# Kernel optimization log

Hardware: AMD Instinct MI355X
Metric: run time of the kernel (lower is better)

Reference implementation:

```python
import jax, jax.numpy as jnp
import numpy as np

B, T, I, H = 8192, 658, 7, 1
D1, D2, D3 = 1024, 512, 128


def setup_inputs() -> dict:
    key = jax.random.key(0)
    ks = jax.random.split(key, 14)
    return {
        "x": jax.random.normal(ks[0], (B, T, I), dtype=jnp.float32),
        "h0": jax.random.uniform(ks[1], (1, B, H), dtype=jnp.float32),
        "W_ih": jax.random.normal(ks[2], (H, I), dtype=jnp.float32) * 0.3,
        "W_hh": jax.random.normal(ks[3], (H, H), dtype=jnp.float32) * 0.3,
        "b_ih": jax.random.normal(ks[4], (H,), dtype=jnp.float32) * 0.1,
        "b_hh": jax.random.normal(ks[5], (H,), dtype=jnp.float32) * 0.1,
        "w1": jax.random.normal(ks[6], (D1, T), dtype=jnp.float32) * 0.03,
        "b1": jax.random.normal(ks[7], (D1,), dtype=jnp.float32) * 0.01,
        "w2": jax.random.normal(ks[8], (D2, D1), dtype=jnp.float32) * 0.03,
        "b2": jax.random.normal(ks[9], (D2,), dtype=jnp.float32) * 0.01,
        "w3": jax.random.normal(ks[10], (D3, D2), dtype=jnp.float32) * 0.03,
        "b3": jax.random.normal(ks[11], (D3,), dtype=jnp.float32) * 0.01,
        "w4": jax.random.normal(ks[12], (T, D3), dtype=jnp.float32) * 0.03,
        "b4": jax.random.normal(ks[13], (T,), dtype=jnp.float32) * 0.01,
    }


def _forward(x, h0, W_ih, W_hh, b_ih, b_hh, w1, b1, w2, b2, w3, b3, w4, b4):
    # Precompute input projection for all timesteps: [T, B, H]
    xw = jnp.einsum("bti,hi->tbh", x, W_ih) + b_ih

    def step(h, xw_t):  # h: [B, H]
        h_new = jnp.tanh(xw_t + h @ W_hh.T + b_hh)
        return h_new, h_new

    h_last, hs = jax.lax.scan(step, h0[0], xw)  # hs: [T, B, H]
    out = jnp.transpose(hs, (1, 0, 2)).reshape(-1, T)  # [B, T] (view(-1, seq))

    out = jax.nn.relu(out @ w1.T + b1)
    out = jax.nn.relu(out @ w2.T + b2)
    out = jax.nn.relu(out @ w3.T + b3)
    out = out @ w4.T + b4
    return out, h_last[None]  # hidden: [1, B, H]


def reference(x, h0, W_ih, W_hh, b_ih, b_hh, w1, b1, w2, b2, w3, b3, w4, b4):
    return _forward(x, h0, W_ih, W_hh, b_ih, b_hh, w1, b1, w2, b2, w3, b3, w4, b4)
```

## Files before the change

### kernel.cpp

```cpp
#include <hip/hip_runtime.h>
#include <hip/hip_bf16.h>
#include <stdint.h>
#include <stddef.h>

#define B_  8192
#define T_  658
#define I_  7
#define TP  672
#define D1_ 1024
#define D2_ 512
#define D3_ 128
#define NP4 768

#define NB  64
#define CT  32
#define NCH 21

#define XWBLKS 21504
#define CVBLKS 5376

typedef __bf16 bf16x8 __attribute__((ext_vector_type(8)));
typedef float  floatx4 __attribute__((ext_vector_type(4)));

__device__ __forceinline__ void gload_lds16(const void* g, void* l) {
    __builtin_amdgcn_global_load_lds(
        (const __attribute__((address_space(1))) void*)g,
        (__attribute__((address_space(3))) void*)l, 16, 0, 0);
}

__device__ __forceinline__ unsigned int pack_bf16x2(float a, float b) {
    unsigned int ua = __float_as_uint(a);
    unsigned int ub = __float_as_uint(b);
    ua += 0x7fffu + ((ua >> 16) & 1u);
    ub += 0x7fffu + ((ub >> 16) & 1u);
    return (ua >> 16) | (ub & 0xffff0000u);
}

__device__ __forceinline__ float bf16lo(unsigned int u) { return __uint_as_float(u << 16); }
__device__ __forceinline__ float bf16hi(unsigned int u) { return __uint_as_float(u & 0xffff0000u); }

__global__ void xw_conv_kernel(const float* __restrict__ x,
                               const float* __restrict__ Wih,
                               const float* __restrict__ bih,
                               __bf16* __restrict__ xwb,
                               const float* __restrict__ w1, const float* __restrict__ w2,
                               const float* __restrict__ w3, const float* __restrict__ w4,
                               __bf16* __restrict__ w1b, __bf16* __restrict__ w2b,
                               __bf16* __restrict__ w3b, __bf16* __restrict__ w4b) {
    if (blockIdx.x < XWBLKS) {
        const int i = blockIdx.x * 256 + threadIdx.x;
        const int b = i / TP, t = i - b * TP;
        float s = 0.0f;
        if (t < T_) {
            const float* xp = x + ((size_t)b * T_ + t) * I_;
            s = bih[0];
#pragma unroll
            for (int j = 0; j < I_; ++j) s = fmaf(xp[j], Wih[j], s);
        }
        xwb[i] = (__bf16)s;
        return;
    }
    int i = (blockIdx.x - XWBLKS) * 256 + threadIdx.x;
    if (i < D1_ * TP) {
        int r = i / TP, c = i - r * TP;
        w1b[i] = (__bf16)(c < T_ ? w1[r * T_ + c] : 0.0f);
        return;
    }
    i -= D1_ * TP;
    if (i < D2_ * D1_) { w2b[i] = (__bf16)w2[i]; return; }
    i -= D2_ * D1_;
    if (i < D3_ * D2_) { w3b[i] = (__bf16)w3[i]; return; }
    i -= D3_ * D2_;
    {
        int r = i / D3_, c = i - r * D3_;
        w4b[i] = (__bf16)(r < T_ ? w4[r * D3_ + c] : 0.0f);
    }
}

__global__ __launch_bounds__(64) void scan_kernel(
    const __bf16* __restrict__ xwb, const float* __restrict__ h0,
    const float* __restrict__ Whh, const float* __restrict__ bhh,
    __bf16* __restrict__ A0, float* __restrict__ hlast) {
    __shared__ float        lds_x[CT * (NB + 1)];
    __shared__ unsigned int lds_o[NB * 17];

    const int tid = threadIdx.x;
    const int b0 = blockIdx.x * NB;
    const float whh = Whh[0], bh = bhh[0];
    const float C2L = 2.8853900817779268f;
    const float whhc = whh * C2L;
    float h = h0[b0 + tid];

    uint4 pf[4];
    unsigned int res[CT / 2];

#pragma unroll
    for (int l = 0; l < 4; ++l) {
        const int idx = l * NB + tid;
        const int bl = idx >> 2, q = idx & 3;
        pf[l] = *(const uint4*)(xwb + (size_t)(b0 + bl) * TP + q * 8);
    }

    for (int c = 0; c < NCH; ++c) {
        const int t0 = c * CT;
        __syncthreads();
#pragma unroll
        for (int l = 0; l < 4; ++l) {
            const int idx = l * NB + tid;
            const int bl = idx >> 2, q = idx & 3;
            const uint4 v = pf[l];
            lds_x[(q * 8 + 0) * (NB + 1) + bl] = bf16lo(v.x);
            lds_x[(q * 8 + 1) * (NB + 1) + bl] = bf16hi(v.x);
            lds_x[(q * 8 + 2) * (NB + 1) + bl] = bf16lo(v.y);
            lds_x[(q * 8 + 3) * (NB + 1) + bl] = bf16hi(v.y);
            lds_x[(q * 8 + 4) * (NB + 1) + bl] = bf16lo(v.z);
            lds_x[(q * 8 + 5) * (NB + 1) + bl] = bf16hi(v.z);
            lds_x[(q * 8 + 6) * (NB + 1) + bl] = bf16lo(v.w);
            lds_x[(q * 8 + 7) * (NB + 1) + bl] = bf16hi(v.w);
        }
        if (c > 0) {
#pragma unroll
            for (int j = 0; j < 16; ++j) lds_o[tid * 17 + j] = res[j];
        }
        __syncthreads();
        if (c > 0) {
            const int tprev = t0 - CT;
#pragma unroll
            for (int l = 0; l < 4; ++l) {
                const int idx = l * NB + tid;
                const int bl = idx >> 2, q = idx & 3;
                uint4 v;
                v.x = lds_o[bl * 17 + q * 4 + 0];
                v.y = lds_o[bl * 17 + q * 4 + 1];
                v.z = lds_o[bl * 17 + q * 4 + 2];
                v.w = lds_o[bl * 17 + q * 4 + 3];
                *(uint4*)(A0 + (size_t)(b0 + bl) * TP + tprev + q * 8) = v;
            }
        }
        if (c + 1 < NCH) {
            const int tn = t0 + CT;
#pragma unroll
            for (int l = 0; l < 4; ++l) {
                const int idx = l * NB + tid;
                const int bl = idx >> 2, q = idx & 3;
                pf[l] = *(const uint4*)(xwb + (size_t)(b0 + bl) * TP + tn + q * 8);
            }
        }
        if (c < NCH - 1) {
#pragma unroll
            for (int k = 0; k < CT; k += 2) {
                float xv0 = lds_x[k * (NB + 1) + tid];
                float xv1 = lds_x[(k + 1) * (NB + 1) + tid];
                float e0 = __builtin_amdgcn_exp2f(fmaf(h, whhc, (xv0 + bh) * C2L));
                h = fmaf(-2.0f, __builtin_amdgcn_rcpf(e0 + 1.0f), 1.0f);
                float r0 = h;
                float e1 = __builtin_amdgcn_exp2f(fmaf(h, whhc, (xv1 + bh) * C2L));
                h = fmaf(-2.0f, __builtin_amdgcn_rcpf(e1 + 1.0f), 1.0f);
                res[k >> 1] = pack_bf16x2(r0, h);
            }
        } else {
            const int nval = T_ - t0;
#pragma unroll
            for (int k = 0; k < CT; k += 2) {
                float r0 = 0.0f, r1 = 0.0f;
                if (k < nval) {
                    float xv0 = lds_x[k * (NB + 1) + tid];
                    float e0 = __builtin_amdgcn_exp2f(fmaf(h, whhc, (xv0 + bh) * C2L));
                    h = fmaf(-2.0f, __builtin_amdgcn_rcpf(e0 + 1.0f), 1.0f);
                    r0 = h;
                }
                if (k + 1 < nval) {
                    float xv1 = lds_x[(k + 1) * (NB + 1) + tid];
                    float e1 = __builtin_amdgcn_exp2f(fmaf(h, whhc, (xv1 + bh) * C2L));
                    h = fmaf(-2.0f, __builtin_amdgcn_rcpf(e1 + 1.0f), 1.0f);
                    r1 = h;
                }
                res[k >> 1] = pack_bf16x2(r0, r1);
            }
        }
    }
    __syncthreads();
#pragma unroll
    for (int j = 0; j < 16; ++j) lds_o[tid * 17 + j] = res[j];
    __syncthreads();
    {
        const int tprev = TP - CT;
#pragma unroll
        for (int l = 0; l < 4; ++l) {
            const int idx = l * NB + tid;
            const int bl = idx >> 2, q = idx & 3;
            uint4 v;
            v.x = lds_o[bl * 17 + q * 4 + 0];
            v.y = lds_o[bl * 17 + q * 4 + 1];
            v.z = lds_o[bl * 17 + q * 4 + 2];
            v.w = lds_o[bl * 17 + q * 4 + 3];
            *(uint4*)(A0 + (size_t)(b0 + bl) * TP + tprev + q * 8) = v;
        }
    }
    hlast[b0 + tid] = h;
}

template<int BM, int BN>
__global__ __launch_bounds__(256, 4) void gemm_bt(
    const __bf16* __restrict__ A, const __bf16* __restrict__ W,
    const float* __restrict__ bias, __bf16* __restrict__ outb,
    float* __restrict__ outf, int K, int Npad, int Nreal, int relu) {
    constexpr int MI = BM / 32;
    constexpr int NJ = BN / 32;
    constexpr int nA = BM / 64;
    constexpr int nB = BN / 64;
    __shared__ __align__(16) __bf16 As[BM * 32];
    __shared__ __align__(16) __bf16 Bs[BN * 32];

    const int tid = threadIdx.x;
    const int m0 = blockIdx.x * BM, n0 = blockIdx.y * BN;
    const int lane = tid & 63, wave = tid >> 6;
    const int wm = (wave & 1) * (BM / 2), wn = (wave >> 1) * (BN / 2);
    const int quad = lane >> 4, l16 = lane & 15;

    const int eoff = tid * 8;
    const int rowS = eoff >> 5;
    const int colS = eoff & 31;
    const __bf16* gaa[nA];
    const __bf16* gbb[nB];
    __bf16* laa[nA];
    __bf16* lbb[nB];
#pragma unroll
    for (int c = 0; c < nA; ++c) {
        gaa[c] = A + (size_t)(m0 + rowS + c * 64) * K + colS;
        laa[c] = As + c * 2048 + (tid & 192) * 8;
    }
#pragma unroll
    for (int c = 0; c < nB; ++c) {
        gbb[c] = W + (size_t)(n0 + rowS + c * 64) * K + colS;
        lbb[c] = Bs + c * 2048 + (tid & 192) * 8;
    }

    floatx4 acc[MI][NJ] = {};

    for (int k0 = 0; k0 < K; k0 += 32) {
#pragma unroll
        for (int c = 0; c < nA; ++c) gload_lds16(gaa[c] + k0, laa[c]);
#pragma unroll
        for (int c = 0; c < nB; ++c) gload_lds16(gbb[c] + k0, lbb[c]);
        __syncthreads();

        bf16x8 af[MI], bg[NJ];
#pragma unroll
        for (int i = 0; i < MI; ++i)
            af[i] = *(const bf16x8*)(As + (wm + i * 16 + l16) * 32 + quad * 8);
#pragma unroll
        for (int j = 0; j < NJ; ++j)
            bg[j] = *(const bf16x8*)(Bs + (wn + j * 16 + l16) * 32 + quad * 8);
#pragma unroll
        for (int i = 0; i < MI; ++i)
#pragma unroll
            for (int j = 0; j < NJ; ++j)
                acc[i][j] = __builtin_amdgcn_mfma_f32_16x16x32_bf16(af[i], bg[j], acc[i][j], 0, 0, 0);
        __syncthreads();
    }

#pragma unroll
    for (int j = 0; j < NJ; ++j) {
        const int n = n0 + wn + j * 16 + l16;
        const float bv = (n < Nreal) ? bias[n] : 0.0f;
#pragma unroll
        for (int i = 0; i < MI; ++i) {
#pragma unroll
            for (int r = 0; r < 4; ++r) {
                const int m = m0 + wm + i * 16 + quad * 4 + r;
                float v = acc[i][j][r] + bv;
                if (relu) v = fmaxf(v, 0.0f);
                if (outb) {
                    outb[(size_t)m * Npad + n] = (__bf16)v;
                } else if (n < Nreal) {
                    outf[(size_t)m * Nreal + n] = v;
                }
            }
        }
    }
}

extern "C" void kernel_launch(void* const* d_in, const int* in_sizes, int n_in,
                              void* d_out, int out_size, void* d_ws, size_t ws_size,
                              hipStream_t stream) {
    const float* x   = (const float*)d_in[0];
    const float* h0  = (const float*)d_in[1];
    const float* Wih = (const float*)d_in[2];
    const float* Whh = (const float*)d_in[3];
    const float* bih = (const float*)d_in[4];
    const float* bhh = (const float*)d_in[5];
    const float* w1  = (const float*)d_in[6];
    const float* b1  = (const float*)d_in[7];
    const float* w2  = (const float*)d_in[8];
    const float* b2  = (const float*)d_in[9];
    const float* w3  = (const float*)d_in[10];
    const float* b3  = (const float*)d_in[11];
    const float* w4  = (const float*)d_in[12];
    const float* b4  = (const float*)d_in[13];
    float* out = (float*)d_out;
    char* ws = (char*)d_ws;

    __bf16* w1b = (__bf16*)(ws + 0);
    __bf16* w2b = (__bf16*)(ws + 1376256);
    __bf16* w3b = (__bf16*)(ws + 2424832);
    __bf16* w4b = (__bf16*)(ws + 2555904);
    __bf16* A0  = (__bf16*)(ws + 2752512);
    __bf16* A1  = (__bf16*)(ws + 13762560);
    __bf16* A2  = (__bf16*)(ws + 30539776);
    __bf16* A3  = (__bf16*)(ws + 38928384);
    __bf16* xwb = (__bf16*)(ws + 13762560);

    xw_conv_kernel<<<XWBLKS + CVBLKS, 256, 0, stream>>>(
        x, Wih, bih, xwb, w1, w2, w3, w4, w1b, w2b, w3b, w4b);
    scan_kernel<<<128, 64, 0, stream>>>(xwb, h0, Whh, bhh, A0, out + (size_t)B_ * T_);

    gemm_bt<64,128><<<dim3(128, 8), 256, 0, stream>>>(A0, w1b, b1, A1, nullptr, TP,  D1_, D1_, 1);
    gemm_bt<64,64> <<<dim3(128, 8), 256, 0, stream>>>(A1, w2b, b2, A2, nullptr, D1_, D2_, D2_, 1);
    gemm_bt<64,64> <<<dim3(128, 2), 256, 0, stream>>>(A2, w3b, b3, A3, nullptr, D2_, D3_, D3_, 1);
    gemm_bt<64,128><<<dim3(128, 6), 256, 0, stream>>>(A3, w4b, b4, nullptr, out, D3_, NP4, T_, 0);
}
```

Baseline: 333.0 us.

## Shorten scan recurrence chain, remap GEMM blocks per XCD, enlarge GEMM tiles

The scan recurrence now carries r = (1-h)/2 instead of h. Each step becomes fma, exp2, add, rcp, which removes one dependent op from the serial critical path. The GEMM kernel remaps block IDs so that consecutive M-tiles land on the same XCD for L2 reuse. The first two GEMMs use 128-row tiles with adjusted launch-bounds occupancy hints, which means fewer blocks and more reuse per block but possibly lower occupancy.

```diff
diff --git a/kernel.cpp b/kernel.cpp
--- a/kernel.cpp
+++ b/kernel.cpp
@@ -89,7 +89,9 @@
     const float whh = Whh[0], bh = bhh[0];
     const float C2L = 2.8853900817779268f;
     const float whhc = whh * C2L;
+    const float m2w = -2.0f * whhc;
     float h = h0[b0 + tid];
+    float r = (1.0f - h) * 0.5f;
 
     uint4 pf[4];
     unsigned int res[CT / 2];
@@ -151,12 +153,13 @@
             for (int k = 0; k < CT; k += 2) {
                 float xv0 = lds_x[k * (NB + 1) + tid];
                 float xv1 = lds_x[(k + 1) * (NB + 1) + tid];
-                float e0 = __builtin_amdgcn_exp2f(fmaf(h, whhc, (xv0 + bh) * C2L));
-                h = fmaf(-2.0f, __builtin_amdgcn_rcpf(e0 + 1.0f), 1.0f);
-                float r0 = h;
-                float e1 = __builtin_amdgcn_exp2f(fmaf(h, whhc, (xv1 + bh) * C2L));
-                h = fmaf(-2.0f, __builtin_amdgcn_rcpf(e1 + 1.0f), 1.0f);
-                res[k >> 1] = pack_bf16x2(r0, h);
+                float c0 = fmaf(xv0 + bh, C2L, whhc);
+                float c1 = fmaf(xv1 + bh, C2L, whhc);
+                r = __builtin_amdgcn_rcpf(__builtin_amdgcn_exp2f(fmaf(m2w, r, c0)) + 1.0f);
+                float h0v = fmaf(-2.0f, r, 1.0f);
+                r = __builtin_amdgcn_rcpf(__builtin_amdgcn_exp2f(fmaf(m2w, r, c1)) + 1.0f);
+                h = fmaf(-2.0f, r, 1.0f);
+                res[k >> 1] = pack_bf16x2(h0v, h);
             }
         } else {
             const int nval = T_ - t0;
@@ -165,14 +168,16 @@
                 float r0 = 0.0f, r1 = 0.0f;
                 if (k < nval) {
                     float xv0 = lds_x[k * (NB + 1) + tid];
-                    float e0 = __builtin_amdgcn_exp2f(fmaf(h, whhc, (xv0 + bh) * C2L));
-                    h = fmaf(-2.0f, __builtin_amdgcn_rcpf(e0 + 1.0f), 1.0f);
+                    r = __builtin_amdgcn_rcpf(
+                        __builtin_amdgcn_exp2f(fmaf(m2w, r, fmaf(xv0 + bh, C2L, whhc))) + 1.0f);
+                    h = fmaf(-2.0f, r, 1.0f);
                     r0 = h;
                 }
                 if (k + 1 < nval) {
                     float xv1 = lds_x[(k + 1) * (NB + 1) + tid];
-                    float e1 = __builtin_amdgcn_exp2f(fmaf(h, whhc, (xv1 + bh) * C2L));
-                    h = fmaf(-2.0f, __builtin_amdgcn_rcpf(e1 + 1.0f), 1.0f);
+                    r = __builtin_amdgcn_rcpf(
+                        __builtin_amdgcn_exp2f(fmaf(m2w, r, fmaf(xv1 + bh, C2L, whhc))) + 1.0f);
+                    h = fmaf(-2.0f, r, 1.0f);
                     r1 = h;
                 }
                 res[k >> 1] = pack_bf16x2(r0, r1);
@@ -200,8 +205,8 @@
     hlast[b0 + tid] = h;
 }
 
-template<int BM, int BN>
-__global__ __launch_bounds__(256, 4) void gemm_bt(
+template<int BM, int BN, int MINW>
+__global__ __launch_bounds__(256, MINW) void gemm_bt(
     const __bf16* __restrict__ A, const __bf16* __restrict__ W,
     const float* __restrict__ bias, __bf16* __restrict__ outb,
     float* __restrict__ outf, int K, int Npad, int Nreal, int relu) {
@@ -213,7 +218,20 @@
     __shared__ __align__(16) __bf16 Bs[BN * 32];
 
     const int tid = threadIdx.x;
-    const int m0 = blockIdx.x * BM, n0 = blockIdx.y * BN;
+    int mb, nb;
+    {
+        const int nbx = gridDim.x;
+        const int bid = blockIdx.y * nbx + blockIdx.x;
+        if ((nbx & 7) == 0) {
+            const int mpx = nbx >> 3;
+            const int xcd = bid & 7, j = bid >> 3;
+            mb = xcd * mpx + (j % mpx);
+            nb = j / mpx;
+        } else {
+            mb = blockIdx.x; nb = blockIdx.y;
+        }
+    }
+    const int m0 = mb * BM, n0 = nb * BN;
     const int lane = tid & 63, wave = tid >> 6;
     const int wm = (wave & 1) * (BM / 2), wn = (wave >> 1) * (BN / 2);
     const int quad = lane >> 4, l16 = lane & 15;
@@ -315,8 +333,8 @@
         x, Wih, bih, xwb, w1, w2, w3, w4, w1b, w2b, w3b, w4b);
     scan_kernel<<<128, 64, 0, stream>>>(xwb, h0, Whh, bhh, A0, out + (size_t)B_ * T_);
 
-    gemm_bt<64,128><<<dim3(128, 8), 256, 0, stream>>>(A0, w1b, b1, A1, nullptr, TP,  D1_, D1_, 1);
-    gemm_bt<64,64> <<<dim3(128, 8), 256, 0, stream>>>(A1, w2b, b2, A2, nullptr, D1_, D2_, D2_, 1);
-    gemm_bt<64,64> <<<dim3(128, 2), 256, 0, stream>>>(A2, w3b, b3, A3, nullptr, D2_, D3_, D3_, 1);
-    gemm_bt<64,128><<<dim3(128, 6), 256, 0, stream>>>(A3, w4b, b4, nullptr, out, D3_, NP4, T_, 0);
-}
+    gemm_bt<128,128,2><<<dim3(64, 8), 256, 0, stream>>>(A0, w1b, b1, A1, nullptr, TP,  D1_, D1_, 1);
+    gemm_bt<128,64,4> <<<dim3(64, 8), 256, 0, stream>>>(A1, w2b, b2, A2, nullptr, D1_, D2_, D2_, 1);
+    gemm_bt<64,64,4>  <<<dim3(128, 2), 256, 0, stream>>>(A2, w3b, b3, A3, nullptr, D2_, D3_, D3_, 1);
+    gemm_bt<64,128,4> <<<dim3(128, 6), 256, 0, stream>>>(A3, w4b, b4, nullptr, out, D3_, NP4, T_, 0);
+}
```

Measured after the change: 336.1 us. Within noise of the previous version (+0.9%).
